# Kernel optimization log

Hardware: AMD Instinct MI355X
Metric: run time of the kernel (lower is better)

Reference implementation:

```python
import jax, jax.numpy as jnp
import numpy as np

D_MODEL = 1024
NUM_HEADS = 16
D_K = D_MODEL // NUM_HEADS


def setup_inputs() -> dict:
    key = jax.random.key(0)
    k1, k2, k3, kq, kk, kv, ko = jax.random.split(key, 7)
    B, S = 4, 2048
    scale = 1.0 / np.sqrt(D_MODEL)
    return {
        "Q_in": jax.random.normal(k1, (B, S, D_MODEL), dtype=jnp.float32),
        "K_in": jax.random.normal(k2, (B, S, D_MODEL), dtype=jnp.float32),
        "V_in": jax.random.normal(k3, (B, S, D_MODEL), dtype=jnp.float32),
        "W_q": jax.random.normal(kq, (D_MODEL, D_MODEL), dtype=jnp.float32) * scale,
        "W_k": jax.random.normal(kk, (D_MODEL, D_MODEL), dtype=jnp.float32) * scale,
        "W_v": jax.random.normal(kv, (D_MODEL, D_MODEL), dtype=jnp.float32) * scale,
        "W_o": jax.random.normal(ko, (D_MODEL, D_MODEL), dtype=jnp.float32) * scale,
    }


def _split_heads(x):
    B, S, _ = x.shape
    return x.reshape(B, S, NUM_HEADS, D_K).transpose(0, 2, 1, 3)  # [B,H,S,d_k]


def reference(Q_in, K_in, V_in, W_q, W_k, W_v, W_o):
    # nn.Linear: y = x @ W.T ; here W_* stored as [out, in] equivalent square,
    # use x @ W.T convention to match torch.
    Q = _split_heads(Q_in @ W_q.T)
    K = _split_heads(K_in @ W_k.T)
    V = _split_heads(V_in @ W_v.T)
    scores = jnp.einsum("bhqd,bhkd->bhqk", Q, K) / jnp.sqrt(jnp.float32(D_K))
    attn = jax.nn.softmax(scores, axis=-1)  # [B,H,S,S]
    out = jnp.einsum("bhqk,bhkd->bhqd", attn, V)
    B, H, S, dk = out.shape
    concat = out.transpose(0, 2, 1, 3).reshape(B, S, H * dk)
    return concat @ W_o.T
```

## Files before the change

kernel.cpp:

```cpp
#include <hip/hip_runtime.h>
#include <math.h>

typedef __bf16 bf16x8v __attribute__((ext_vector_type(8)));
typedef float f32x4 __attribute__((ext_vector_type(4)));
typedef float f32x16 __attribute__((ext_vector_type(16)));

__device__ __forceinline__ void async_copy16(void* lds, const void* g) {
  __builtin_amdgcn_global_load_lds(
      (const __attribute__((address_space(1))) void*)g,
      (__attribute__((address_space(3))) void*)lds, 16, 0, 0);
}

struct CastArgs {
  const float* s[7];
  __bf16* d[7];
};
__global__ __launch_bounds__(256) void cast_kernel(CastArgs a) {
  const int t = blockIdx.y;
  const int n = (t < 3) ? 8388608 : 1048576;
  const int i = (blockIdx.x * 256 + threadIdx.x) * 8;
  if (i >= n) return;
  const float4 v0 = *(const float4*)(a.s[t] + i);
  const float4 v1 = *(const float4*)(a.s[t] + i + 4);
  bf16x8v o;
  o[0] = (__bf16)v0.x; o[1] = (__bf16)v0.y; o[2] = (__bf16)v0.z; o[3] = (__bf16)v0.w;
  o[4] = (__bf16)v1.x; o[5] = (__bf16)v1.y; o[6] = (__bf16)v1.z; o[7] = (__bf16)v1.w;
  *(bf16x8v*)(a.d[t] + i) = o;
}

template <int MODE, typename OutT>
__global__ __launch_bounds__(256) void gemm_bt(const __bf16* A, const __bf16* B,
                                               OutT* C,
                                               const __bf16* A2, const __bf16* B2,
                                               OutT* C2,
                                               int M, int N, int K) {
  __shared__ __bf16 As[128 * 64];
  __shared__ __bf16 Bs[128 * 64];
  if (blockIdx.z == 1) { A = A2; B = B2; C = C2; }
  const int tid = threadIdx.x;
  const int wave = tid >> 6, lane = tid & 63;
  const int lgrp = lane >> 4, lmod = lane & 15;
  const int bm = (MODE == 3 ? blockIdx.y : blockIdx.x) * 128;
  const int bn = (MODE == 3 ? blockIdx.x : blockIdx.y) * 128;
  const int wm = (wave >> 1) * 64, wn = (wave & 1) * 64;

  f32x4 acc[4][4];
#pragma unroll
  for (int mi = 0; mi < 4; mi++)
#pragma unroll
    for (int ni = 0; ni < 4; ni++)
#pragma unroll
      for (int r = 0; r < 4; r++) acc[mi][ni][r] = 0.f;

  for (int kt = 0; kt < K; kt += 64) {
#pragma unroll
    for (int i = 0; i < 4; i++) {
      const int s = i * 256 + tid;
      const int r = s >> 3, cb = s & 7;
      const int gc = (cb ^ (r & 7)) * 8;
      async_copy16(&As[s * 8], &A[(size_t)(bm + r) * K + kt + gc]);
      async_copy16(&Bs[s * 8], &B[(size_t)(bn + r) * K + kt + gc]);
    }
    __syncthreads();
#pragma unroll
    for (int ks = 0; ks < 2; ks++) {
      bf16x8v af[4], bf[4];
#pragma unroll
      for (int mi = 0; mi < 4; mi++) {
        const int row = wm + mi * 16 + lmod;
        af[mi] = *(const bf16x8v*)&As[row * 64 + ((ks * 4 + lgrp) ^ (row & 7)) * 8];
      }
#pragma unroll
      for (int ni = 0; ni < 4; ni++) {
        const int row = wn + ni * 16 + lmod;
        bf[ni] = *(const bf16x8v*)&Bs[row * 64 + ((ks * 4 + lgrp) ^ (row & 7)) * 8];
      }
#pragma unroll
      for (int mi = 0; mi < 4; mi++)
#pragma unroll
        for (int ni = 0; ni < 4; ni++)
          acc[mi][ni] = __builtin_amdgcn_mfma_f32_16x16x32_bf16(af[mi], bf[ni],
                                                                acc[mi][ni], 0, 0, 0);
    }
    __syncthreads();
  }

#pragma unroll
  for (int mi = 0; mi < 4; mi++)
#pragma unroll
    for (int ni = 0; ni < 4; ni++)
#pragma unroll
      for (int r = 0; r < 4; r++) {
        const int row = bm + wm + mi * 16 + lgrp * 4 + r;
        const int col = bn + wn + ni * 16 + lmod;
        if (MODE == 0) {
          C[(size_t)row * N + col] = (OutT)acc[mi][ni][r];
        } else if (MODE == 1) {
          C[(size_t)(row >> 11) * 2097152 + (size_t)(col >> 6) * 131072 +
            (size_t)(row & 2047) * 64 + (col & 63)] = (OutT)acc[mi][ni][r];
        } else {
          C[(size_t)(col >> 11) * 2097152 + (size_t)(row >> 6) * 131072 +
            (size_t)(row & 63) * 2048 + (col & 2047)] = (OutT)acc[mi][ni][r];
        }
      }
}

__global__ __launch_bounds__(256) void attn_kernel(const __bf16* __restrict__ Qh,
                                                   const __bf16* __restrict__ Kh,
                                                   const __bf16* __restrict__ Vt,
                                                   __bf16* __restrict__ O) {
  __shared__ __bf16 Ks[128 * 64];
  __shared__ __bf16 Vts[64 * 128];

  const int tid = threadIdx.x;
  const int wave = tid >> 6, lane = tid & 63;
  const int l31 = lane & 31, hi = lane >> 5;
  const int qt = blockIdx.y, y = blockIdx.x;
  const size_t hb = (size_t)y * 131072;
  const __bf16* Qb = Qh + hb + (size_t)qt * 128 * 64;
  const __bf16* Kb = Kh + hb;
  const __bf16* Vb = Vt + hb;
  const int wq0 = wave * 32;

  const float qscale = 0.125f * 1.44269504f;
  bf16x8v qf[4];
#pragma unroll
  for (int ks = 0; ks < 4; ks++) {
    bf16x8v q = *(const bf16x8v*)&Qb[(wq0 + l31) * 64 + ks * 16 + hi * 8];
#pragma unroll
    for (int j = 0; j < 8; j++) q[j] = (__bf16)((float)q[j] * qscale);
    qf[ks] = q;
  }

  float m_run = -INFINITY;
  float l_run = 0.f;
  f32x16 oacc[2];
#pragma unroll
  for (int nd = 0; nd < 2; nd++)
#pragma unroll
    for (int r = 0; r < 16; r++) oacc[nd][r] = 0.f;

  for (int kv0 = 0; kv0 < 2048; kv0 += 128) {
#pragma unroll
    for (int i = 0; i < 4; i++) {
      const int s = i * 256 + tid;
      {
        const int r = s >> 3, cb = s & 7;
        async_copy16(&Ks[s * 8], &Kb[(size_t)(kv0 + r) * 64 + (cb ^ (r & 7)) * 8]);
      }
      {
        const int r = s >> 4, cb = s & 15;
        async_copy16(&Vts[s * 8], &Vb[(size_t)r * 2048 + kv0 + (cb ^ (r & 7)) * 8]);
      }
    }
    __syncthreads();

#pragma unroll 1
    for (int half = 0; half < 2; half++) {
      f32x16 st[2];
#pragma unroll
      for (int kvt = 0; kvt < 2; kvt++)
#pragma unroll
        for (int r = 0; r < 16; r++) st[kvt][r] = 0.f;
#pragma unroll
      for (int ks = 0; ks < 4; ks++) {
        const int sl = ((ks * 2 + hi) ^ (l31 & 7)) * 8;
        const bf16x8v kf0 =
            *(const bf16x8v*)&Ks[(half * 64 + l31) * 64 + sl];
        const bf16x8v kf1 =
            *(const bf16x8v*)&Ks[(half * 64 + 32 + l31) * 64 + sl];
        __builtin_amdgcn_s_setprio(1);
        st[0] = __builtin_amdgcn_mfma_f32_32x32x16_bf16(kf0, qf[ks], st[0], 0, 0, 0);
        st[1] = __builtin_amdgcn_mfma_f32_32x32x16_bf16(kf1, qf[ks], st[1], 0, 0, 0);
        __builtin_amdgcn_s_setprio(0);
      }

      float b[16];
#pragma unroll
      for (int j = 0; j < 16; j++) b[j] = fmaxf(st[0][j], st[1][j]);
#pragma unroll
      for (int s = 8; s > 0; s >>= 1)
#pragma unroll
        for (int j = 0; j < 8; j++)
          if (j < s) b[j] = fmaxf(b[j], b[j + s]);
      float rmax = b[0];
      rmax = fmaxf(rmax, __shfl_xor(rmax, 32));

      if (!__all(rmax - m_run <= 8.f)) {
        const float mnew = fmaxf(m_run, rmax);
        const float alpha = __builtin_amdgcn_exp2f(m_run - mnew);
        m_run = mnew;
        l_run *= alpha;
#pragma unroll
        for (int r = 0; r < 16; r++) {
          const float ar = __shfl(alpha, (r & 3) + 8 * (r >> 2) + 4 * hi);
          oacc[0][r] *= ar;
          oacc[1][r] *= ar;
        }
      }

      float psum = 0.f;
#pragma unroll
      for (int kvt = 0; kvt < 2; kvt++) {
#pragma unroll
        for (int sub = 0; sub < 2; sub++) {
          const int ks2 = kvt * 2 + sub;
          const int vs = ((half * 8 + ks2 * 2 + hi) ^ (l31 & 7)) * 8;
          const bf16x8v vf0 = *(const bf16x8v*)&Vts[l31 * 128 + vs];
          const bf16x8v vf1 = *(const bf16x8v*)&Vts[(32 + l31) * 128 + vs];
          const int o = sub * 8;
          float p[8];
#pragma unroll
          for (int j = 0; j < 8; j++) {
            p[j] = __builtin_amdgcn_exp2f(st[kvt][o + j] - m_run);
            psum += p[j];
          }
          unsigned x0, y0, x1, y1;
          asm("v_cvt_pk_bf16_f32 %0, %1, %2" : "=v"(x0) : "v"(p[0]), "v"(p[1]));
          asm("v_cvt_pk_bf16_f32 %0, %1, %2" : "=v"(y0) : "v"(p[4]), "v"(p[5]));
          asm("v_cvt_pk_bf16_f32 %0, %1, %2" : "=v"(x1) : "v"(p[2]), "v"(p[3]));
          asm("v_cvt_pk_bf16_f32 %0, %1, %2" : "=v"(y1) : "v"(p[6]), "v"(p[7]));
          asm("v_permlane32_swap_b32 %0, %1" : "+v"(x0), "+v"(y0));
          asm("v_permlane32_swap_b32 %0, %1" : "+v"(x1), "+v"(y1));
          union { unsigned u[4]; bf16x8v v; } af;
          af.u[0] = x0; af.u[1] = x1; af.u[2] = y0; af.u[3] = y1;
          __builtin_amdgcn_s_setprio(1);
          oacc[0] = __builtin_amdgcn_mfma_f32_32x32x16_bf16(af.v, vf0, oacc[0], 0, 0, 0);
          oacc[1] = __builtin_amdgcn_mfma_f32_32x32x16_bf16(af.v, vf1, oacc[1], 0, 0, 0);
          __builtin_amdgcn_s_setprio(0);
        }
      }
      l_run += psum;
    }
    __syncthreads();
  }

  l_run += __shfl_xor(l_run, 32);
  const float linv = 1.f / l_run;
  const int b = y >> 4, h = y & 15;
#pragma unroll
  for (int r = 0; r < 16; r++) {
    const int q = (r & 3) + 8 * (r >> 2) + 4 * hi;
    const float inv = __shfl(linv, q);
    const int srow = qt * 128 + wq0 + q;
    const size_t base = ((size_t)(b * 2048 + srow)) * 1024 + h * 64;
    O[base + l31] = (__bf16)(oacc[0][r] * inv);
    O[base + 32 + l31] = (__bf16)(oacc[1][r] * inv);
  }
}

extern "C" void kernel_launch(void* const* d_in, const int* in_sizes, int n_in,
                              void* d_out, int out_size, void* d_ws, size_t ws_size,
                              hipStream_t stream) {
  const float* Qin = (const float*)d_in[0];
  const float* Kin = (const float*)d_in[1];
  const float* Vin = (const float*)d_in[2];
  const float* Wq = (const float*)d_in[3];
  const float* Wk = (const float*)d_in[4];
  const float* Wv = (const float*)d_in[5];
  const float* Wo = (const float*)d_in[6];
  float* out = (float*)d_out;

  __bf16* base = (__bf16*)d_ws;
  __bf16* Qbf = base;
  __bf16* Kbf = base + 8388608;
  __bf16* Vbf = base + 16777216;
  __bf16* Wqb = base + 25165824;
  __bf16* Wkb = base + 26214400;
  __bf16* Wvb = base + 27262976;
  __bf16* Wob = base + 28311552;
  __bf16* Qh = base + 29360128;
  __bf16* Kh = base + 37748736;
  __bf16* Vt = base + 46137344;
  __bf16* AO = Qbf;

  CastArgs ca;
  ca.s[0] = Qin; ca.s[1] = Kin; ca.s[2] = Vin;
  ca.s[3] = Wq;  ca.s[4] = Wk;  ca.s[5] = Wv;  ca.s[6] = Wo;
  ca.d[0] = Qbf; ca.d[1] = Kbf; ca.d[2] = Vbf;
  ca.d[3] = Wqb; ca.d[4] = Wkb; ca.d[5] = Wvb; ca.d[6] = Wob;
  cast_kernel<<<dim3(4096, 7), 256, 0, stream>>>(ca);

  const int M = 8192, N = 1024, K = 1024;
  dim3 bb(256);
  gemm_bt<1, __bf16><<<dim3(64, 8, 2), bb, 0, stream>>>(Qbf, Wqb, Qh,
                                                        Kbf, Wkb, Kh, M, N, K);
  gemm_bt<3, __bf16><<<dim3(64, 8), bb, 0, stream>>>(Wvb, Vbf, Vt,
                                                     nullptr, nullptr, nullptr,
                                                     1024, 8192, K);
  attn_kernel<<<dim3(64, 16), bb, 0, stream>>>(Qh, Kh, Vt, AO);
  gemm_bt<0, float><<<dim3(64, 8), bb, 0, stream>>>(AO, Wob, out,
                                                    nullptr, nullptr, nullptr,
                                                    M, N, K);
}
```

Measured before the change: 376.6 us.

## Double-buffer K/V tiles in attention kernel with 64-row prefetch

The attention loop now uses two 64-key LDS buffers for K and V and issues the async global-to-LDS copies for the next tile before computing the current one. Before, each 128-key tile was loaded and then waited on by a barrier before any compute could start. The aim is to hide global load latency behind the MFMA and softmax work. In exchange the tile is smaller, so there are twice as many iterations and barriers. The only barrier is at the end of each iteration, which may not guarantee the prefetched data has landed before it is read.

```diff
diff --git a/kernel.cpp b/kernel.cpp
--- a/kernel.cpp
+++ b/kernel.cpp
@@ -109,8 +109,8 @@
                                                    const __bf16* __restrict__ Kh,
                                                    const __bf16* __restrict__ Vt,
                                                    __bf16* __restrict__ O) {
-  __shared__ __bf16 Ks[128 * 64];
-  __shared__ __bf16 Vts[64 * 128];
+  __shared__ __bf16 Ks[2][64 * 64];
+  __shared__ __bf16 Vts[2][64 * 64];
 
   const int tid = threadIdx.x;
   const int wave = tid >> 6, lane = tid & 63;
@@ -122,6 +122,11 @@
   const __bf16* Vb = Vt + hb;
   const int wq0 = wave * 32;
 
+  const int s0 = tid, s1 = 256 + tid;
+  const int kr0 = s0 >> 3, kc0 = s0 & 7;
+  const int kr1 = s1 >> 3, kc1 = s1 & 7;
+  const int vr0 = kr0, vc0 = kc0, vr1 = kr1, vc1 = kc1;
+
   const float qscale = 0.125f * 1.44269504f;
   bf16x8v qf[4];
 #pragma unroll
@@ -140,98 +145,99 @@
 #pragma unroll
     for (int r = 0; r < 16; r++) oacc[nd][r] = 0.f;
 
-  for (int kv0 = 0; kv0 < 2048; kv0 += 128) {
-#pragma unroll
-    for (int i = 0; i < 4; i++) {
-      const int s = i * 256 + tid;
-      {
-        const int r = s >> 3, cb = s & 7;
-        async_copy16(&Ks[s * 8], &Kb[(size_t)(kv0 + r) * 64 + (cb ^ (r & 7)) * 8]);
-      }
-      {
-        const int r = s >> 4, cb = s & 15;
-        async_copy16(&Vts[s * 8], &Vb[(size_t)r * 2048 + kv0 + (cb ^ (r & 7)) * 8]);
-      }
-    }
-    __syncthreads();
-
-#pragma unroll 1
-    for (int half = 0; half < 2; half++) {
-      f32x16 st[2];
-#pragma unroll
-      for (int kvt = 0; kvt < 2; kvt++)
-#pragma unroll
-        for (int r = 0; r < 16; r++) st[kvt][r] = 0.f;
-#pragma unroll
-      for (int ks = 0; ks < 4; ks++) {
-        const int sl = ((ks * 2 + hi) ^ (l31 & 7)) * 8;
-        const bf16x8v kf0 =
-            *(const bf16x8v*)&Ks[(half * 64 + l31) * 64 + sl];
-        const bf16x8v kf1 =
-            *(const bf16x8v*)&Ks[(half * 64 + 32 + l31) * 64 + sl];
+  async_copy16(&Ks[0][s0 * 8], &Kb[(size_t)kr0 * 64 + (kc0 ^ (kr0 & 7)) * 8]);
+  async_copy16(&Ks[0][s1 * 8], &Kb[(size_t)kr1 * 64 + (kc1 ^ (kr1 & 7)) * 8]);
+  async_copy16(&Vts[0][s0 * 8], &Vb[(size_t)vr0 * 2048 + (vc0 ^ (vr0 & 7)) * 8]);
+  async_copy16(&Vts[0][s1 * 8], &Vb[(size_t)vr1 * 2048 + (vc1 ^ (vr1 & 7)) * 8]);
+  __syncthreads();
+
+  for (int t = 0; t < 32; t++) {
+    const int bsel = t & 1;
+    if (t < 31) {
+      const int kv1 = (t + 1) * 64;
+      async_copy16(&Ks[bsel ^ 1][s0 * 8],
+                   &Kb[(size_t)(kv1 + kr0) * 64 + (kc0 ^ (kr0 & 7)) * 8]);
+      async_copy16(&Ks[bsel ^ 1][s1 * 8],
+                   &Kb[(size_t)(kv1 + kr1) * 64 + (kc1 ^ (kr1 & 7)) * 8]);
+      async_copy16(&Vts[bsel ^ 1][s0 * 8],
+                   &Vb[(size_t)vr0 * 2048 + kv1 + (vc0 ^ (vr0 & 7)) * 8]);
+      async_copy16(&Vts[bsel ^ 1][s1 * 8],
+                   &Vb[(size_t)vr1 * 2048 + kv1 + (vc1 ^ (vr1 & 7)) * 8]);
+    }
+
+    f32x16 st[2];
+#pragma unroll
+    for (int kvt = 0; kvt < 2; kvt++)
+#pragma unroll
+      for (int r = 0; r < 16; r++) st[kvt][r] = 0.f;
+#pragma unroll
+    for (int ks = 0; ks < 4; ks++) {
+      const int sl = ((ks * 2 + hi) ^ (l31 & 7)) * 8;
+      const bf16x8v kf0 = *(const bf16x8v*)&Ks[bsel][l31 * 64 + sl];
+      const bf16x8v kf1 = *(const bf16x8v*)&Ks[bsel][(32 + l31) * 64 + sl];
+      __builtin_amdgcn_s_setprio(1);
+      st[0] = __builtin_amdgcn_mfma_f32_32x32x16_bf16(kf0, qf[ks], st[0], 0, 0, 0);
+      st[1] = __builtin_amdgcn_mfma_f32_32x32x16_bf16(kf1, qf[ks], st[1], 0, 0, 0);
+      __builtin_amdgcn_s_setprio(0);
+    }
+
+    float bmax[16];
+#pragma unroll
+    for (int j = 0; j < 16; j++) bmax[j] = fmaxf(st[0][j], st[1][j]);
+#pragma unroll
+    for (int s = 8; s > 0; s >>= 1)
+#pragma unroll
+      for (int j = 0; j < 8; j++)
+        if (j < s) bmax[j] = fmaxf(bmax[j], bmax[j + s]);
+    float rmax = bmax[0];
+    rmax = fmaxf(rmax, __shfl_xor(rmax, 32));
+
+    if (!__all(rmax - m_run <= 8.f)) {
+      const float mnew = fmaxf(m_run, rmax);
+      const float alpha = __builtin_amdgcn_exp2f(m_run - mnew);
+      m_run = mnew;
+      l_run *= alpha;
+#pragma unroll
+      for (int r = 0; r < 16; r++) {
+        const float ar = __shfl(alpha, (r & 3) + 8 * (r >> 2) + 4 * hi);
+        oacc[0][r] *= ar;
+        oacc[1][r] *= ar;
+      }
+    }
+
+    float psum = 0.f;
+#pragma unroll
+    for (int kvt = 0; kvt < 2; kvt++) {
+#pragma unroll
+      for (int sub = 0; sub < 2; sub++) {
+        const int ks2 = kvt * 2 + sub;
+        const int vs = ((ks2 * 2 + hi) ^ (l31 & 7)) * 8;
+        const bf16x8v vf0 = *(const bf16x8v*)&Vts[bsel][l31 * 64 + vs];
+        const bf16x8v vf1 = *(const bf16x8v*)&Vts[bsel][(32 + l31) * 64 + vs];
+        const int o = sub * 8;
+        float p[8];
+#pragma unroll
+        for (int j = 0; j < 8; j++) {
+          p[j] = __builtin_amdgcn_exp2f(st[kvt][o + j] - m_run);
+          psum += p[j];
+        }
+        unsigned x0, y0, x1, y1;
+        asm("v_cvt_pk_bf16_f32 %0, %1, %2" : "=v"(x0) : "v"(p[0]), "v"(p[1]));
+        asm("v_cvt_pk_bf16_f32 %0, %1, %2" : "=v"(y0) : "v"(p[4]), "v"(p[5]));
+        asm("v_cvt_pk_bf16_f32 %0, %1, %2" : "=v"(x1) : "v"(p[2]), "v"(p[3]));
+        asm("v_cvt_pk_bf16_f32 %0, %1, %2" : "=v"(y1) : "v"(p[6]), "v"(p[7]));
+        asm("v_permlane32_swap_b32 %0, %1" : "+v"(x0), "+v"(y0));
+        asm("v_permlane32_swap_b32 %0, %1" : "+v"(x1), "+v"(y1));
+        union { unsigned u[4]; bf16x8v v; } af;
+        af.u[0] = x0; af.u[1] = x1; af.u[2] = y0; af.u[3] = y1;
         __builtin_amdgcn_s_setprio(1);
-        st[0] = __builtin_amdgcn_mfma_f32_32x32x16_bf16(kf0, qf[ks], st[0], 0, 0, 0);
-        st[1] = __builtin_amdgcn_mfma_f32_32x32x16_bf16(kf1, qf[ks], st[1], 0, 0, 0);
+        oacc[0] = __builtin_amdgcn_mfma_f32_32x32x16_bf16(af.v, vf0, oacc[0], 0, 0, 0);
+        oacc[1] = __builtin_amdgcn_mfma_f32_32x32x16_bf16(af.v, vf1, oacc[1], 0, 0, 0);
         __builtin_amdgcn_s_setprio(0);
       }
-
-      float b[16];
-#pragma unroll
-      for (int j = 0; j < 16; j++) b[j] = fmaxf(st[0][j], st[1][j]);
-#pragma unroll
-      for (int s = 8; s > 0; s >>= 1)
-#pragma unroll
-        for (int j = 0; j < 8; j++)
-          if (j < s) b[j] = fmaxf(b[j], b[j + s]);
-      float rmax = b[0];
-      rmax = fmaxf(rmax, __shfl_xor(rmax, 32));
-
-      if (!__all(rmax - m_run <= 8.f)) {
-        const float mnew = fmaxf(m_run, rmax);
-        const float alpha = __builtin_amdgcn_exp2f(m_run - mnew);
-        m_run = mnew;
-        l_run *= alpha;
-#pragma unroll
-        for (int r = 0; r < 16; r++) {
-          const float ar = __shfl(alpha, (r & 3) + 8 * (r >> 2) + 4 * hi);
-          oacc[0][r] *= ar;
-          oacc[1][r] *= ar;
-        }
-      }
-
-      float psum = 0.f;
-#pragma unroll
-      for (int kvt = 0; kvt < 2; kvt++) {
-#pragma unroll
-        for (int sub = 0; sub < 2; sub++) {
-          const int ks2 = kvt * 2 + sub;
-          const int vs = ((half * 8 + ks2 * 2 + hi) ^ (l31 & 7)) * 8;
-          const bf16x8v vf0 = *(const bf16x8v*)&Vts[l31 * 128 + vs];
-          const bf16x8v vf1 = *(const bf16x8v*)&Vts[(32 + l31) * 128 + vs];
-          const int o = sub * 8;
-          float p[8];
-#pragma unroll
-          for (int j = 0; j < 8; j++) {
-            p[j] = __builtin_amdgcn_exp2f(st[kvt][o + j] - m_run);
-            psum += p[j];
-          }
-          unsigned x0, y0, x1, y1;
-          asm("v_cvt_pk_bf16_f32 %0, %1, %2" : "=v"(x0) : "v"(p[0]), "v"(p[1]));
-          asm("v_cvt_pk_bf16_f32 %0, %1, %2" : "=v"(y0) : "v"(p[4]), "v"(p[5]));
-          asm("v_cvt_pk_bf16_f32 %0, %1, %2" : "=v"(x1) : "v"(p[2]), "v"(p[3]));
-          asm("v_cvt_pk_bf16_f32 %0, %1, %2" : "=v"(y1) : "v"(p[6]), "v"(p[7]));
-          asm("v_permlane32_swap_b32 %0, %1" : "+v"(x0), "+v"(y0));
-          asm("v_permlane32_swap_b32 %0, %1" : "+v"(x1), "+v"(y1));
-          union { unsigned u[4]; bf16x8v v; } af;
-          af.u[0] = x0; af.u[1] = x1; af.u[2] = y0; af.u[3] = y1;
-          __builtin_amdgcn_s_setprio(1);
-          oacc[0] = __builtin_amdgcn_mfma_f32_32x32x16_bf16(af.v, vf0, oacc[0], 0, 0, 0);
-          oacc[1] = __builtin_amdgcn_mfma_f32_32x32x16_bf16(af.v, vf1, oacc[1], 0, 0, 0);
-          __builtin_amdgcn_s_setprio(0);
-        }
-      }
-      l_run += psum;
-    }
+    }
+    l_run += psum;
+
     __syncthreads();
   }
 
```

After: 370.6 us. Within noise of the previous version (-1.6%).
